# Performance work log

Measured on AMD Instinct MI355X. Metric: run time of the kernel, lower is better.

## Reference

```python
import jax, jax.numpy as jnp
import numpy as np

BLOCK = 512  # circulant block size

def block_circulant_matmul(x, w):
    """Block-circulant linear layer (CirCNN-style), no bias.
    x: (..., p*BLOCK); w: (q, p, BLOCK) -> out: (..., q*BLOCK).
    Each (q,p) block is a circulant matrix applied via FFT (circular conv).
    """
    q, p, b = w.shape
    xb = x.reshape(x.shape[:-1] + (p, b))            # (..., p, b)
    Xf = jnp.fft.rfft(xb, axis=-1)                    # (..., p, b//2+1) complex
    Wf = jnp.fft.rfft(w, axis=-1)                     # (q, p, b//2+1)
    Yf = jnp.einsum('...pf,qpf->...qf', Xf, Wf)       # sum over input blocks
    y = jnp.fft.irfft(Yf, n=b, axis=-1)               # (..., q, b)
    return y.reshape(x.shape[:-1] + (q * b,))

def setup_inputs() -> dict:
    key = jax.random.key(0)
    k1, k2, k3, k4 = jax.random.split(key, 4)
    d_model, d_ff, b = 2048, 5632, BLOCK
    p_in, q_ff = d_model // b, d_ff // b              # 4, 11
    scale = 1.0 / np.sqrt(d_model)
    x = jax.random.normal(k1, (4, 4096, d_model), dtype=jnp.float32)
    w_gate = jax.random.normal(k2, (q_ff, p_in, b), dtype=jnp.float32) * scale
    w_up   = jax.random.normal(k3, (q_ff, p_in, b), dtype=jnp.float32) * scale
    w_down = jax.random.normal(k4, (p_in, q_ff, b), dtype=jnp.float32) * (1.0 / np.sqrt(d_ff))
    return {"x": x, "w_gate": w_gate, "w_up": w_up, "w_down": w_down}

def reference(x, w_gate, w_up, w_down):
    # SwiGLU: down( SiLU(gate(x)) * up(x) ); dropout=0 -> identity
    gate = jax.nn.silu(block_circulant_matmul(x, w_gate))
    up = block_circulant_matmul(x, w_up)
    return block_circulant_matmul(gate * up, w_down)
```

## Files before the change

### kernel.cpp

```cpp
#include <hip/hip_runtime.h>
#include <math.h>


__device__ __forceinline__ int swz(int n) { return n ^ ((n >> 3) & 15); }

struct Tw { float t0r[7], t0i[7], t1r[7], t1i[7]; };

__device__ __forceinline__ void make_tw(int l, Tw& T)
{
    float c0, s0;
    __sincosf(-6.283185307179586f * (float)l * (1.0f/512.0f), &s0, &c0);
    float pr = c0, pi = s0;
    T.t0r[0] = pr; T.t0i[0] = pi;
#pragma unroll
    for (int m = 1; m < 7; ++m) {
        float nr = pr*c0 - pi*s0, ni = pr*s0 + pi*c0;
        pr = nr; pi = ni;
        T.t0r[m] = pr; T.t0i[m] = pi;
    }
    float c1, s1;
    __sincosf(-6.283185307179586f * (float)(l >> 3) * (1.0f/64.0f), &s1, &c1);
    pr = c1; pi = s1;
    T.t1r[0] = pr; T.t1i[0] = pi;
#pragma unroll
    for (int m = 1; m < 7; ++m) {
        float nr = pr*c1 - pi*s1, ni = pr*s1 + pi*c1;
        pr = nr; pi = ni;
        T.t1r[m] = pr; T.t1i[m] = pi;
    }
}

template<bool INV>
__device__ __forceinline__ void dft8(float xr[8], float xi[8])
{
    const float C = 0.70710678118654752f;
    float tr[4], ti[4], ur[4], ui[4];
#pragma unroll
    for (int q = 0; q < 4; ++q) {
        tr[q] = xr[q] + xr[q+4];  ti[q] = xi[q] + xi[q+4];
        ur[q] = xr[q] - xr[q+4];  ui[q] = xi[q] - xi[q+4];
    }
    {
        float xx = ur[1], yy = ui[1];
        if (!INV) { ur[1] = C*(xx+yy); ui[1] = C*(yy-xx); }
        else      { ur[1] = C*(xx-yy); ui[1] = C*(xx+yy); }
    }
    {
        float xx = ur[2], yy = ui[2];
        if (!INV) { ur[2] = yy;  ui[2] = -xx; }
        else      { ur[2] = -yy; ui[2] = xx; }
    }
    {
        float xx = ur[3], yy = ui[3];
        if (!INV) { ur[3] = C*(yy-xx);  ui[3] = -C*(xx+yy); }
        else      { ur[3] = -C*(xx+yy); ui[3] = C*(xx-yy); }
    }
    {
        float s0r=tr[0]+tr[2], s0i=ti[0]+ti[2];
        float d0r=tr[0]-tr[2], d0i=ti[0]-ti[2];
        float s1r=tr[1]+tr[3], s1i=ti[1]+ti[3];
        float e1r=tr[1]-tr[3], e1i=ti[1]-ti[3];
        float d1r, d1i;
        if (!INV) { d1r = e1i;  d1i = -e1r; } else { d1r = -e1i; d1i = e1r; }
        xr[0]=s0r+s1r; xi[0]=s0i+s1i;
        xr[2]=d0r+d1r; xi[2]=d0i+d1i;
        xr[4]=s0r-s1r; xi[4]=s0i-s1i;
        xr[6]=d0r-d1r; xi[6]=d0i-d1i;
    }
    {
        float s0r=ur[0]+ur[2], s0i=ui[0]+ui[2];
        float d0r=ur[0]-ur[2], d0i=ui[0]-ui[2];
        float s1r=ur[1]+ur[3], s1i=ui[1]+ui[3];
        float e1r=ur[1]-ur[3], e1i=ui[1]-ui[3];
        float d1r, d1i;
        if (!INV) { d1r = e1i;  d1i = -e1r; } else { d1r = -e1i; d1i = e1r; }
        xr[1]=s0r+s1r; xi[1]=s0i+s1i;
        xr[3]=d0r+d1r; xi[3]=d0i+d1i;
        xr[5]=s0r-s1r; xi[5]=s0i-s1i;
        xr[7]=d0r-d1r; xi[7]=d0i-d1i;
    }
}

template<bool INV>
__device__ __forceinline__ void fft512_r8(float2* wk, int l, const Tw& T)
{
    float xr[8], xi[8];
#pragma unroll
    for (int q = 0; q < 8; ++q) { float2 v = wk[swz(l + 64*q)]; xr[q]=v.x; xi[q]=v.y; }
    dft8<INV>(xr, xi);
#pragma unroll
    for (int m = 1; m < 8; ++m) {
        float wr = T.t0r[m-1], wi = INV ? -T.t0i[m-1] : T.t0i[m-1];
        float nr = xr[m]*wr - xi[m]*wi, ni = xr[m]*wi + xi[m]*wr;
        xr[m]=nr; xi[m]=ni;
    }
#pragma unroll
    for (int m = 0; m < 8; ++m) wk[swz(8*l + m)] = make_float2(xr[m], xi[m]);
#pragma unroll
    for (int q = 0; q < 8; ++q) { float2 v = wk[swz(l + 64*q)]; xr[q]=v.x; xi[q]=v.y; }
    dft8<INV>(xr, xi);
#pragma unroll
    for (int m = 1; m < 8; ++m) {
        float wr = T.t1r[m-1], wi = INV ? -T.t1i[m-1] : T.t1i[m-1];
        float nr = xr[m]*wr - xi[m]*wi, ni = xr[m]*wi + xi[m]*wr;
        xr[m]=nr; xi[m]=ni;
    }
    {
        const int base = 64*(l>>3) + (l&7);
#pragma unroll
        for (int m = 0; m < 8; ++m) wk[swz(base + 8*m)] = make_float2(xr[m], xi[m]);
    }
#pragma unroll
    for (int q = 0; q < 8; ++q) { float2 v = wk[swz(l + 64*q)]; xr[q]=v.x; xi[q]=v.y; }
    dft8<INV>(xr, xi);
#pragma unroll
    for (int m = 0; m < 8; ++m) wk[swz(l + 64*m)] = make_float2(xr[m], xi[m]);
}

__global__ __launch_bounds__(64) void wf_prep(const float* __restrict__ wg,
                                              const float* __restrict__ wu,
                                              const float* __restrict__ wd,
                                              float2* __restrict__ wsp)
{
    __shared__ float2 wk[512];
    const int t = threadIdx.x;
    Tw T; make_tw(t, T);
    const int b = blockIdx.x;
    const float* src = (b < 44) ? (wg + (size_t)b * 512)
                     : (b < 88) ? (wu + (size_t)(b - 44) * 512)
                                : (wd + (size_t)(b - 88) * 512);
    float2* dst = wsp + (size_t)b * 257;

#pragma unroll
    for (int i = 0; i < 8; ++i) { int n = t + 64*i; wk[swz(n)] = make_float2(src[n], 0.f); }
    fft512_r8<false>(wk, t, T);
    const float sc = 1.0f / 512.0f;
#pragma unroll
    for (int i = 0; i < 5; ++i) {
        int k = t + 64*i;
        if (k <= 256) { float2 z = wk[swz(k)]; dst[k] = make_float2(sc*z.x, sc*z.y); }
    }
}

__global__ __launch_bounds__(256) void bcffn(const float* __restrict__ x,
                                             const float2* __restrict__ wsp,
                                             float* __restrict__ out)
{
    __shared__ float2 sWork[4 * 512];
    __shared__ float2 sXf[4][257];
    __shared__ float2 sHf[11][257];

    const int tid = threadIdx.x;
    const int t = tid & 63, w = tid >> 6;
    const size_t row = blockIdx.x;

    Tw T; make_tw(t, T);

    const float2* Wg = wsp;
    const float2* Wu = wsp + 44 * 257;
    const float2* Wd = wsp + 88 * 257;

    float2* wk = sWork + (w << 9);

    if (w < 2) {
        const float4* xa = (const float4*)(x + row * 2048 + (size_t)(2*w)   * 512);
        const float4* xb = (const float4*)(x + row * 2048 + (size_t)(2*w+1) * 512);
#pragma unroll
        for (int u = 0; u < 2; ++u) {
            int e = t + 64*u;
            float4 a = xa[e], b = xb[e];
            int n = 4*e;
            wk[swz(n+0)] = make_float2(a.x, b.x);
            wk[swz(n+1)] = make_float2(a.y, b.y);
            wk[swz(n+2)] = make_float2(a.z, b.z);
            wk[swz(n+3)] = make_float2(a.w, b.w);
        }
        fft512_r8<false>(wk, t, T);
#pragma unroll
        for (int u = 0; u < 5; ++u) {
            int k = t + 64*u;
            if (k <= 256) {
                float2 z = wk[swz(k)], m = wk[swz((512 - k) & 511)];
                sXf[2*w][k]   = make_float2(0.5f*(z.x + m.x), 0.5f*(z.y - m.y));
                sXf[2*w+1][k] = make_float2(0.5f*(z.y + m.y), 0.5f*(m.x - z.x));
            }
        }
    }
    __syncthreads();

    auto einsum_gu = [&](int q) {
#pragma unroll
        for (int u = 0; u < 5; ++u) {
            int k = t + 64*u;
            if (k <= 256) {
                float gr=0.f, gi=0.f, ur_=0.f, ui_=0.f;
#pragma unroll
                for (int p = 0; p < 4; ++p) {
                    float2 X = sXf[p][k];
                    float2 a = Wg[(q*4 + p)*257 + k];
                    float2 b = Wu[(q*4 + p)*257 + k];
                    gr  += X.x*a.x - X.y*a.y;  gi  += X.x*a.y + X.y*a.x;
                    ur_ += X.x*b.x - X.y*b.y;  ui_ += X.x*b.y + X.y*b.x;
                }
                wk[swz(k)] = make_float2(gr - ui_, gi + ur_);
                if (k != 0 && k != 256)
                    wk[swz(512 - k)] = make_float2(gr + ui_, ur_ - gi);
            }
        }
    };

    {
        const int qa = w, qb = w + 4;
        float ha[8];

        einsum_gu(qa);
        fft512_r8<true>(wk, t, T);
#pragma unroll
        for (int u = 0; u < 8; ++u) {
            float2 v = wk[swz(t + 64*u)];
            ha[u] = v.x * v.y / (1.f + __expf(-v.x));
        }

        einsum_gu(qb);
        fft512_r8<true>(wk, t, T);
#pragma unroll
        for (int u = 0; u < 8; ++u) {
            int n = t + 64*u;
            float2 v = wk[swz(n)];
            float hb = v.x * v.y / (1.f + __expf(-v.x));
            wk[swz(n)] = make_float2(ha[u], hb);
        }
        fft512_r8<false>(wk, t, T);
#pragma unroll
        for (int u = 0; u < 5; ++u) {
            int k = t + 64*u;
            if (k <= 256) {
                float2 z = wk[swz(k)], m = wk[swz((512 - k) & 511)];
                sHf[qa][k] = make_float2(0.5f*(z.x + m.x), 0.5f*(z.y - m.y));
                sHf[qb][k] = make_float2(0.5f*(z.y + m.y), 0.5f*(m.x - z.x));
            }
        }

        if (w < 3) {
            const int qc = w + 8;
            einsum_gu(qc);
            fft512_r8<true>(wk, t, T);
#pragma unroll
            for (int u = 0; u < 8; ++u) {
                int n = t + 64*u;
                float2 v = wk[swz(n)];
                wk[swz(n)] = make_float2(v.x * v.y / (1.f + __expf(-v.x)), 0.f);
            }
            fft512_r8<false>(wk, t, T);
#pragma unroll
            for (int u = 0; u < 5; ++u) {
                int k = t + 64*u;
                if (k <= 256) sHf[qc][k] = wk[swz(k)];
            }
        }
    }
    __syncthreads();

    float Zr[5] = {0.f,0.f,0.f,0.f,0.f};
    float Zi[5] = {0.f,0.f,0.f,0.f,0.f};
#pragma unroll
    for (int u = 0; u < 5; ++u) {
        int k = t + 64*u;
        if (k <= 256) {
            float zr = 0.f, zi = 0.f;
#pragma unroll
            for (int q = 0; q < 11; ++q) {
                float2 H = sHf[q][k];
                float2 d = Wd[(w*11 + q)*257 + k];
                zr += H.x*d.x - H.y*d.y;
                zi += H.x*d.y + H.y*d.x;
            }
            Zr[u] = zr; Zi[u] = zi;
        }
    }
    if (w >= 2) {
#pragma unroll
        for (int u = 0; u < 5; ++u) {
            int k = t + 64*u;
            if (k <= 256) sXf[w-2][k] = make_float2(Zr[u], Zi[u]);
        }
    }
    __syncthreads();
    if (w < 2) {
#pragma unroll
        for (int u = 0; u < 5; ++u) {
            int k = t + 64*u;
            if (k <= 256) {
                float2 zb = sXf[w][k];
                wk[swz(k)] = make_float2(Zr[u] - zb.y, Zi[u] + zb.x);
                if (k != 0 && k != 256)
                    wk[swz(512 - k)] = make_float2(Zr[u] + zb.y, zb.x - Zi[u]);
            }
        }
        fft512_r8<true>(wk, t, T);
        float4* oa = (float4*)(out + row * 2048 + (size_t)w       * 512);
        float4* ob = (float4*)(out + row * 2048 + (size_t)(w + 2) * 512);
#pragma unroll
        for (int u = 0; u < 2; ++u) {
            int e = t + 64*u, n = 4*e;
            float2 v0 = wk[swz(n)],   v1 = wk[swz(n+1)];
            float2 v2 = wk[swz(n+2)], v3 = wk[swz(n+3)];
            oa[e] = make_float4(v0.x, v1.x, v2.x, v3.x);
            ob[e] = make_float4(v0.y, v1.y, v2.y, v3.y);
        }
    }
}

extern "C" void kernel_launch(void* const* d_in, const int* in_sizes, int n_in,
                              void* d_out, int out_size, void* d_ws, size_t ws_size,
                              hipStream_t stream)
{
    (void)n_in; (void)out_size; (void)ws_size;
    const float* x  = (const float*)d_in[0];
    const float* wg = (const float*)d_in[1];
    const float* wu = (const float*)d_in[2];
    const float* wd = (const float*)d_in[3];
    float2* wsp = (float2*)d_ws;
    float*  out = (float*)d_out;

    const int rows = in_sizes[0] / 2048;

    wf_prep<<<132, 64, 0, stream>>>(wg, wu, wd, wsp);
    bcffn<<<rows, 256, 0, stream>>>(x, wsp, out);
}
```

Before: 549.6 us.

## Process each row with a single wavefront and stream down-projection accumulation

The fused block-circulant SwiGLU kernel moves from four wavefronts per row to one 64-thread wavefront that handles all gate/up pairs sequentially. The down-projection einsum now accumulates into registers right after each hidden spectrum pair is produced, which removes the 11x257 hidden-spectrum shared buffer and every __syncthreads. The aim is to cut LDS footprint and barrier stalls so more blocks fit per CU. The cost is a longer serial chain per block and 40 extra accumulator registers per thread, which may raise register pressure.

```diff
diff --git a/kernel.cpp b/kernel.cpp
--- a/kernel.cpp
+++ b/kernel.cpp
@@ -142,16 +142,14 @@
     }
 }
 
-__global__ __launch_bounds__(256) void bcffn(const float* __restrict__ x,
-                                             const float2* __restrict__ wsp,
-                                             float* __restrict__ out)
-{
-    __shared__ float2 sWork[4 * 512];
+__global__ __launch_bounds__(64) void bcffn(const float* __restrict__ x,
+                                            const float2* __restrict__ wsp,
+                                            float* __restrict__ out)
+{
+    __shared__ float2 wk[512];
     __shared__ float2 sXf[4][257];
-    __shared__ float2 sHf[11][257];
-
-    const int tid = threadIdx.x;
-    const int t = tid & 63, w = tid >> 6;
+
+    const int t = threadIdx.x;
     const size_t row = blockIdx.x;
 
     Tw T; make_tw(t, T);
@@ -160,11 +158,10 @@
     const float2* Wu = wsp + 44 * 257;
     const float2* Wd = wsp + 88 * 257;
 
-    float2* wk = sWork + (w << 9);
-
-    if (w < 2) {
-        const float4* xa = (const float4*)(x + row * 2048 + (size_t)(2*w)   * 512);
-        const float4* xb = (const float4*)(x + row * 2048 + (size_t)(2*w+1) * 512);
+#pragma unroll 1
+    for (int h = 0; h < 2; ++h) {
+        const float4* xa = (const float4*)(x + row * 2048 + (size_t)(2*h)   * 512);
+        const float4* xb = (const float4*)(x + row * 2048 + (size_t)(2*h+1) * 512);
 #pragma unroll
         for (int u = 0; u < 2; ++u) {
             int e = t + 64*u;
@@ -181,12 +178,11 @@
             int k = t + 64*u;
             if (k <= 256) {
                 float2 z = wk[swz(k)], m = wk[swz((512 - k) & 511)];
-                sXf[2*w][k]   = make_float2(0.5f*(z.x + m.x), 0.5f*(z.y - m.y));
-                sXf[2*w+1][k] = make_float2(0.5f*(z.y + m.y), 0.5f*(m.x - z.x));
-            }
-        }
-    }
-    __syncthreads();
+                sXf[2*h][k]   = make_float2(0.5f*(z.x + m.x), 0.5f*(z.y - m.y));
+                sXf[2*h+1][k] = make_float2(0.5f*(z.y + m.y), 0.5f*(m.x - z.x));
+            }
+        }
+    }
 
     auto einsum_gu = [&](int q) {
 #pragma unroll
@@ -209,10 +205,12 @@
         }
     };
 
-    {
-        const int qa = w, qb = w + 4;
-        float ha[8];
-
+    float Zr[4][5] = {{0.f}}, Zi[4][5] = {{0.f}};
+    float ha[8];
+
+#pragma unroll 1
+    for (int pr = 0; pr < 6; ++pr) {
+        const int qa = 2 * pr;
         einsum_gu(qa);
         fft512_r8<true>(wk, t, T);
 #pragma unroll
@@ -220,86 +218,71 @@
             float2 v = wk[swz(t + 64*u)];
             ha[u] = v.x * v.y / (1.f + __expf(-v.x));
         }
-
-        einsum_gu(qb);
-        fft512_r8<true>(wk, t, T);
-#pragma unroll
-        for (int u = 0; u < 8; ++u) {
-            int n = t + 64*u;
-            float2 v = wk[swz(n)];
-            float hb = v.x * v.y / (1.f + __expf(-v.x));
-            wk[swz(n)] = make_float2(ha[u], hb);
-        }
-        fft512_r8<false>(wk, t, T);
+        if (pr < 5) {
+            const int qb = qa + 1;
+            einsum_gu(qb);
+            fft512_r8<true>(wk, t, T);
+#pragma unroll
+            for (int u = 0; u < 8; ++u) {
+                int n = t + 64*u;
+                float2 v = wk[swz(n)];
+                float hb = v.x * v.y / (1.f + __expf(-v.x));
+                wk[swz(n)] = make_float2(ha[u], hb);
+            }
+            fft512_r8<false>(wk, t, T);
+#pragma unroll
+            for (int u = 0; u < 5; ++u) {
+                int k = t + 64*u;
+                if (k <= 256) {
+                    float2 z = wk[swz(k)], m = wk[swz((512 - k) & 511)];
+                    float Har = 0.5f*(z.x + m.x), Hai = 0.5f*(z.y - m.y);
+                    float Hbr = 0.5f*(z.y + m.y), Hbi = 0.5f*(m.x - z.x);
+#pragma unroll
+                    for (int p = 0; p < 4; ++p) {
+                        float2 da = Wd[(p*11 + qa)*257 + k];
+                        float2 db = Wd[(p*11 + qb)*257 + k];
+                        Zr[p][u] += Har*da.x - Hai*da.y + Hbr*db.x - Hbi*db.y;
+                        Zi[p][u] += Har*da.y + Hai*da.x + Hbr*db.y + Hbi*db.x;
+                    }
+                }
+            }
+        } else {
+#pragma unroll
+            for (int u = 0; u < 8; ++u)
+                wk[swz(t + 64*u)] = make_float2(ha[u], 0.f);
+            fft512_r8<false>(wk, t, T);
+#pragma unroll
+            for (int u = 0; u < 5; ++u) {
+                int k = t + 64*u;
+                if (k <= 256) {
+                    float2 H = wk[swz(k)];
+#pragma unroll
+                    for (int p = 0; p < 4; ++p) {
+                        float2 d = Wd[(p*11 + 10)*257 + k];
+                        Zr[p][u] += H.x*d.x - H.y*d.y;
+                        Zi[p][u] += H.x*d.y + H.y*d.x;
+                    }
+                }
+            }
+        }
+    }
+
+#pragma unroll
+    for (int h = 0; h < 2; ++h) {
+        const int pa = 2*h, pb = 2*h + 1;
 #pragma unroll
         for (int u = 0; u < 5; ++u) {
             int k = t + 64*u;
             if (k <= 256) {
-                float2 z = wk[swz(k)], m = wk[swz((512 - k) & 511)];
-                sHf[qa][k] = make_float2(0.5f*(z.x + m.x), 0.5f*(z.y - m.y));
-                sHf[qb][k] = make_float2(0.5f*(z.y + m.y), 0.5f*(m.x - z.x));
-            }
-        }
-
-        if (w < 3) {
-            const int qc = w + 8;
-            einsum_gu(qc);
-            fft512_r8<true>(wk, t, T);
-#pragma unroll
-            for (int u = 0; u < 8; ++u) {
-                int n = t + 64*u;
-                float2 v = wk[swz(n)];
-                wk[swz(n)] = make_float2(v.x * v.y / (1.f + __expf(-v.x)), 0.f);
-            }
-            fft512_r8<false>(wk, t, T);
-#pragma unroll
-            for (int u = 0; u < 5; ++u) {
-                int k = t + 64*u;
-                if (k <= 256) sHf[qc][k] = wk[swz(k)];
-            }
-        }
-    }
-    __syncthreads();
-
-    float Zr[5] = {0.f,0.f,0.f,0.f,0.f};
-    float Zi[5] = {0.f,0.f,0.f,0.f,0.f};
-#pragma unroll
-    for (int u = 0; u < 5; ++u) {
-        int k = t + 64*u;
-        if (k <= 256) {
-            float zr = 0.f, zi = 0.f;
-#pragma unroll
-            for (int q = 0; q < 11; ++q) {
-                float2 H = sHf[q][k];
-                float2 d = Wd[(w*11 + q)*257 + k];
-                zr += H.x*d.x - H.y*d.y;
-                zi += H.x*d.y + H.y*d.x;
-            }
-            Zr[u] = zr; Zi[u] = zi;
-        }
-    }
-    if (w >= 2) {
-#pragma unroll
-        for (int u = 0; u < 5; ++u) {
-            int k = t + 64*u;
-            if (k <= 256) sXf[w-2][k] = make_float2(Zr[u], Zi[u]);
-        }
-    }
-    __syncthreads();
-    if (w < 2) {
-#pragma unroll
-        for (int u = 0; u < 5; ++u) {
-            int k = t + 64*u;
-            if (k <= 256) {
-                float2 zb = sXf[w][k];
-                wk[swz(k)] = make_float2(Zr[u] - zb.y, Zi[u] + zb.x);
+                wk[swz(k)] = make_float2(Zr[pa][u] - Zi[pb][u], Zi[pa][u] + Zr[pb][u]);
                 if (k != 0 && k != 256)
-                    wk[swz(512 - k)] = make_float2(Zr[u] + zb.y, zb.x - Zi[u]);
+                    wk[swz(512 - k)] = make_float2(Zr[pa][u] + Zi[pb][u],
+                                                   Zr[pb][u] - Zi[pa][u]);
             }
         }
         fft512_r8<true>(wk, t, T);
-        float4* oa = (float4*)(out + row * 2048 + (size_t)w       * 512);
-        float4* ob = (float4*)(out + row * 2048 + (size_t)(w + 2) * 512);
+        float4* oa = (float4*)(out + row * 2048 + (size_t)pa * 512);
+        float4* ob = (float4*)(out + row * 2048 + (size_t)pb * 512);
 #pragma unroll
         for (int u = 0; u < 2; ++u) {
             int e = t + 64*u, n = 4*e;
@@ -326,5 +309,5 @@
     const int rows = in_sizes[0] / 2048;
 
     wf_prep<<<132, 64, 0, stream>>>(wg, wu, wd, wsp);
-    bcffn<<<rows, 256, 0, stream>>>(x, wsp, out);
-}
+    bcffn<<<rows, 64, 0, stream>>>(x, wsp, out);
+}
```

Result: slower. 714.9 us (+30.1%).
